# Kernel tuning notes

Measured on AMD Instinct MI355X. Metric: run time of the kernel, lower is better.

## Reference

```python
import jax, jax.numpy as jnp
import numpy as np

B, C, H = 256, 5, 13
N_AGENTS = 8192
N_EDGES = 262144
ACT = 21


def setup_inputs() -> dict:
    key = jax.random.key(0)
    ks = jax.random.split(key, 20)
    inp = {
        "x": jax.random.normal(ks[0], (B, C, H, H), jnp.float32),
        "x_msg": jax.random.normal(ks[1], (N_AGENTS,), jnp.float32),
        "edge_index": jax.random.randint(ks[2], (N_EDGES, 2), 0, N_AGENTS, jnp.int64 if jax.config.jax_enable_x64 else jnp.int32),
        "action": jax.random.randint(ks[3], (B,), 0, ACT, jnp.int32),
        # params (orthogonal init approximated by scaled normal; math identical)
        "conv1_w": jax.random.normal(ks[4], (32, 5, 3, 3), jnp.float32) * 0.1,
        "conv1_b": jnp.zeros((32,), jnp.float32),
        "conv2_w": jax.random.normal(ks[5], (64, 32, 3, 3), jnp.float32) * 0.05,
        "conv2_b": jnp.zeros((64,), jnp.float32),
        "fc_w": jax.random.normal(ks[6], (512, 1024), jnp.float32) * 0.03,
        "fc_b": jnp.zeros((512,), jnp.float32),
        "fc_mu_w": jax.random.normal(ks[7], (ACT, 512), jnp.float32) * 0.01,
        "fc_mu_b": jnp.zeros((ACT,), jnp.float32),
        "msg_w": jax.random.normal(ks[8], (N_AGENTS, 512), jnp.float32) * 0.01,
        "msg_b": jnp.zeros((N_AGENTS,), jnp.float32),
        "gcn1_w": jax.random.normal(ks[9], (2, 16), jnp.float32) * 0.5,
        "gcn1_b": jnp.zeros((16,), jnp.float32),
        "gcn2_w": jax.random.normal(ks[10], (16, N_AGENTS), jnp.float32) * 0.1,
        "gcn2_b": jnp.zeros((N_AGENTS,), jnp.float32),
    }
    return inp


def _gcn_norm(edge_index, n):
    # add self-loops; edge_index is (E,2) [src, dst]
    loops = jnp.arange(n, dtype=edge_index.dtype)
    src = jnp.concatenate([edge_index[:, 0], loops])
    dst = jnp.concatenate([edge_index[:, 1], loops])
    deg = jax.ops.segment_sum(jnp.ones_like(src, jnp.float32), dst, num_segments=n)
    dinv = jnp.where(deg > 0, jax.lax.rsqrt(deg), 0.0)
    norm = dinv[src] * dinv[dst]  # [E+n]
    return src, dst, norm


def _gcn_conv(h, src, dst, norm, W, b, n):
    hw = h @ W  # [n, out]
    out = jax.ops.segment_sum(norm[:, None] * hw[src], dst, num_segments=n)
    return out + b


def reference(x, x_msg, edge_index, action, conv1_w, conv1_b, conv2_w, conv2_b,
              fc_w, fc_b, fc_mu_w, fc_mu_b, msg_w, msg_b,
              gcn1_w, gcn1_b, gcn2_w, gcn2_b):
    dn = ("NCHW", "OIHW", "NCHW")
    h = jax.lax.conv_general_dilated(x, conv1_w, (2, 2), "VALID", dimension_numbers=dn)
    h = jax.nn.relu(h + conv1_b[None, :, None, None])  # [B,32,6,6]
    h = jax.lax.conv_general_dilated(h, conv2_w, (1, 1), "VALID", dimension_numbers=dn)
    h = jax.nn.relu(h + conv2_b[None, :, None, None])  # [B,64,4,4]
    h = h.reshape(h.shape[0], -1)  # [B,1024], torch NCHW flatten order
    hidden = jax.nn.relu(h @ fc_w.T + fc_b)  # [B,512]

    logits = hidden @ fc_mu_w.T + fc_mu_b            # [B,21]
    actor_encoding = hidden @ msg_w.T + msg_b        # [B,N]

    # Categorical log_prob / entropy for the given action
    logp = jax.nn.log_softmax(logits, axis=-1)
    log_prob = jnp.take_along_axis(logp, action[:, None], axis=1)[:, 0]
    entropy = -jnp.sum(jnp.exp(logp) * logp, axis=-1)

    # GNN message branch (eval mode: dropout is identity)
    feats = jnp.stack([x_msg, actor_encoding[0]], axis=0).T  # [N,2]
    n = feats.shape[0]
    src, dst, norm = _gcn_norm(edge_index, n)
    g = jax.nn.relu(_gcn_conv(feats, src, dst, norm, gcn1_w, gcn1_b, n))  # [N,16]
    g = _gcn_conv(g, src, dst, norm, gcn2_w, gcn2_b, n)                    # [N,N]
    msg_out = jax.nn.log_softmax(g, axis=1).mean(axis=1)                   # [N]

    return (action, msg_out, log_prob, entropy)
```

## Files before the change

kernel.cpp:

```cpp
#include <hip/hip_runtime.h>
#include <hip/hip_bf16.h>

#define NB 256
#define NACT 21
#define NA 8192
#define NE 262144
#define CSR_CAP 128
#define LOG2E 1.44269504f

#if __has_builtin(__builtin_amdgcn_exp2f)
#define EXP2F(x) __builtin_amdgcn_exp2f(x)
#else
#define EXP2F(x) exp2f(x)
#endif

typedef __attribute__((ext_vector_type(8))) short short8;
typedef __attribute__((ext_vector_type(4))) float float4v;

__device__ inline float wsum64(float v) {
#pragma unroll
  for (int m = 32; m > 0; m >>= 1) v += __shfl_xor(v, m, 64);
  return v;
}

__device__ inline unsigned short f2bf(float f) {
  union { __hip_bfloat16 h; unsigned short u; } cv;
  cv.h = __float2bfloat16(f);
  return cv.u;
}

__global__ __launch_bounds__(512, 2) void k_ip(
    const float* __restrict__ x, const float* __restrict__ c1w, const float* __restrict__ c1b_,
    const float* __restrict__ c2w, const float* __restrict__ fcw,
    const float* __restrict__ g2w, const float* __restrict__ g2b,
    unsigned short* c1b, unsigned short* w2abf, int* cnt,
    unsigned short* fcwbf, unsigned short* w2t, float* wpart) {
  __shared__ float sm[3437];
  int t = threadIdx.x, b = blockIdx.x;
  if (b >= 308) {
    float (*red)[17] = (float(*)[17])sm;
    float* b2s = sm + 272;
    int blk = b - 308;
    {
      int base = (blk * 512 + t) * 2;
      float2 v = *(const float2*)&fcw[base];
      fcwbf[base + 0] = f2bf(v.x);
      fcwbf[base + 1] = f2bf(v.y);
    }
    {
      if (t < 256) {
        int jj = t >> 4, k = t & 15;
        int j = blk * 16 + jj;
        float w = g2w[k * 8192 + j];
        w2t[j * 16 + k] = f2bf(w);
        red[jj][k] = w;
      }
      if (t < 16) b2s[t] = g2b[blk * 16 + t];
      __syncthreads();
      if (t < 16) {
        float s = 0.0f;
#pragma unroll
        for (int q = 0; q < 16; q++) s += red[q][t];
        wpart[blk * 17 + t] = s;
      } else if (t == 16) {
        float s = 0.0f;
#pragma unroll
        for (int q = 0; q < 16; q++) s += b2s[q];
        wpart[blk * 17 + 16] = s;
      }
    }
    return;
  }
  if (b >= 272) {
    int i = (b - 272) * 512 + t;
    w2abf[i] = f2bf(c2w[i]);
    return;
  }
  if (b >= 256) {
    cnt[(b - 256) * 512 + t] = 0;
    return;
  }
  float* xs = sm;
  float* w1s = sm + 845;
  float* c1s = sm + 2285;
  for (int i = t; i < 845; i += 512) xs[i] = x[b * 845 + i];
  for (int i = t; i < 1440; i += 512) w1s[i] = c1w[i];
  __syncthreads();
  for (int idx = t; idx < 1152; idx += 512) {
    int oc = idx / 36, p = idx - oc * 36;
    int oy = p / 6, ox = p - oy * 6;
    float acc = c1b_[oc];
    const float* wp = &w1s[oc * 45];
#pragma unroll
    for (int ic = 0; ic < 5; ic++)
#pragma unroll
      for (int ky = 0; ky < 3; ky++)
#pragma unroll
        for (int kx = 0; kx < 3; kx++)
          acc += xs[ic * 169 + (oy * 2 + ky) * 13 + ox * 2 + kx] * wp[ic * 9 + ky * 3 + kx];
    c1s[idx] = fmaxf(acc, 0.0f);
  }
  __syncthreads();
  for (int i = t; i < 4608; i += 512) {
    int p = i / 288, k = i - p * 288;
    int ic = k / 9, r = k - ic * 9;
    int ky = r / 3, kx = r - ky * 3;
    int oy = p >> 2, ox = p & 3;
    c1b[b * 4608 + i] = f2bf(c1s[ic * 36 + (oy + ky) * 6 + ox + kx]);
  }
}

__global__ __launch_bounds__(512, 2) void k_cf(
    const int* __restrict__ edges, int* cnt, int* csr,
    const unsigned short* __restrict__ c1b, const unsigned short* __restrict__ w2abf,
    const float* __restrict__ c2b, const unsigned short* __restrict__ fcwbf,
    const float* __restrict__ fcb, const float* __restrict__ wpart,
    float* hidden, float* wsf) {
  __shared__ __align__(16) unsigned short hs[16384];
  __shared__ __align__(16) unsigned short w2a[18432];
  __shared__ float red[2048];
  int t = threadIdx.x, blk = blockIdx.x;
  int wave = t >> 6, lane = t & 63;
  int m = lane & 15, quad = lane >> 4;
  if (blk >= 1024) {
    if (t < 272) {
      int q = t / 17, c = t - q * 17;
      float s = 0.0f;
      for (int r = q; r < 512; r += 16) s += wpart[r * 17 + c];
      red[t] = s;
    }
    __syncthreads();
    if (t < 17) {
      float s = 0.0f;
#pragma unroll
      for (int q = 0; q < 16; q++) s += red[q * 17 + t];
      wsf[t] = s;
    }
    return;
  }
  if (blk >= 512) {
    int e = (blk - 512) * 512 + t;
    int s = edges[2 * e], d = edges[2 * e + 1];
    int slot = atomicAdd(&cnt[d], 1);
    if (slot < CSR_CAP) csr[d * CSR_CAP + slot] = s;
    return;
  }
  for (int i = t; i < 2304; i += 512)
    *(short8*)&w2a[i * 8] = *(const short8*)&w2abf[i * 8];
  __syncthreads();
  int tr = blk >> 5, tc = blk & 31;
  {
    int nlb = wave * 32;
    int nbase = tr * 256 + nlb;
    float4v z = {0.0f, 0.0f, 0.0f, 0.0f};
    float4v acc00 = z, acc01 = z, acc02 = z, acc03 = z;
    float4v acc10 = z, acc11 = z, acc12 = z, acc13 = z;
#pragma unroll
    for (int ks = 0; ks < 9; ks++) {
      int ko = ks * 32 + quad * 8;
      short8 a0 = *(const short8*)&w2a[(0 * 16 + m) * 288 + ko];
      short8 a1 = *(const short8*)&w2a[(1 * 16 + m) * 288 + ko];
      short8 a2 = *(const short8*)&w2a[(2 * 16 + m) * 288 + ko];
      short8 a3 = *(const short8*)&w2a[(3 * 16 + m) * 288 + ko];
      short8 b0 = *(const short8*)&c1b[(nbase + m) * 288 + ko];
      short8 b1 = *(const short8*)&c1b[(nbase + 16 + m) * 288 + ko];
      acc00 = __builtin_amdgcn_mfma_f32_16x16x32_bf16(a0, b0, acc00, 0, 0, 0);
      acc01 = __builtin_amdgcn_mfma_f32_16x16x32_bf16(a1, b0, acc01, 0, 0, 0);
      acc02 = __builtin_amdgcn_mfma_f32_16x16x32_bf16(a2, b0, acc02, 0, 0, 0);
      acc03 = __builtin_amdgcn_mfma_f32_16x16x32_bf16(a3, b0, acc03, 0, 0, 0);
      acc10 = __builtin_amdgcn_mfma_f32_16x16x32_bf16(a0, b1, acc10, 0, 0, 0);
      acc11 = __builtin_amdgcn_mfma_f32_16x16x32_bf16(a1, b1, acc11, 0, 0, 0);
      acc12 = __builtin_amdgcn_mfma_f32_16x16x32_bf16(a2, b1, acc12, 0, 0, 0);
      acc13 = __builtin_amdgcn_mfma_f32_16x16x32_bf16(a3, b1, acc13, 0, 0, 0);
    }
    float4v accs[2][4] = {{acc00, acc01, acc02, acc03}, {acc10, acc11, acc12, acc13}};
#pragma unroll
    for (int nt = 0; nt < 2; nt++) {
#pragma unroll
      for (int mt = 0; mt < 4; mt++) {
#pragma unroll
        for (int r = 0; r < 4; r++) {
          int oc = mt * 16 + quad * 4 + r;
          int nl = nlb + nt * 16 + m;
          hs[(nl >> 4) * 1024 + oc * 16 + (nl & 15)] =
              f2bf(fmaxf(accs[nt][mt][r] + c2b[oc], 0.0f));
        }
      }
    }
  }
  __syncthreads();
  {
    const unsigned short* ap = &hs[m * 1024 + wave * 128 + quad * 8];
    const unsigned short* bp = &fcwbf[(tc * 16 + m) * 1024 + wave * 128 + quad * 8];
    float4v acc = {0.0f, 0.0f, 0.0f, 0.0f};
#pragma unroll
    for (int ks = 0; ks < 4; ks++) {
      short8 av = *(const short8*)(ap + ks * 32);
      short8 bv = *(const short8*)(bp + ks * 32);
      acc = __builtin_amdgcn_mfma_f32_16x16x32_bf16(av, bv, acc, 0, 0, 0);
    }
#pragma unroll
    for (int r = 0; r < 4; r++) red[wave * 256 + (quad * 4 + r) * 16 + m] = acc[r];
    __syncthreads();
    if (t < 256) {
      float s = 0.0f;
#pragma unroll
      for (int w = 0; w < 8; w++) s += red[w * 256 + t];
      int gr = tr * 16 + (t >> 4);
      int gc = tc * 16 + (t & 15);
      hidden[gr * 512 + gc] = fmaxf(s + fcb[gc], 0.0f);
    }
  }
}

__global__ __launch_bounds__(512, 2) void k_he(
    const float* __restrict__ hidden, const float* __restrict__ muw,
    const float* __restrict__ mub, const float* __restrict__ msgw,
    const float* __restrict__ msgb, const int* __restrict__ cnt,
    const float* __restrict__ x_msg, const int* __restrict__ action,
    float2* xe, float* dinv, float* out) {
  __shared__ float muT[10752];
  __shared__ float hrows[2048];
  int t = threadIdx.x, blk = blockIdx.x;
  int wave = t >> 6, lane = t & 63;
  if (blk >= 512) {
    int i = (blk - 512) * 512 + t;
    float d = rsqrtf((float)cnt[i] + 1.0f);
    dinv[i] = d;
    xe[i].x = d * x_msg[i];
    return;
  }
  if (blk < 64) {
    int b0 = blk * 4;
    for (int i = t; i < 10752; i += 512) {
      int a = i >> 9, k = i & 511;
      muT[k * 21 + a] = muw[i];
    }
    for (int i = t; i < 2048; i += 512) hrows[i] = hidden[b0 * 512 + i];
    __syncthreads();
    if (wave < 4) {
      int b = b0 + wave;
      float logit = -1e30f;
      if (lane < NACT) {
        float acc = mub[lane];
        const float* hr = &hrows[wave * 512];
        for (int k = 0; k < 512; k++) acc += hr[k] * muT[k * 21 + lane];
        logit = acc;
      }
      float mx = logit;
#pragma unroll
      for (int s = 32; s > 0; s >>= 1) mx = fmaxf(mx, __shfl_xor(mx, s, 64));
      float e = (lane < NACT) ? __expf(logit - mx) : 0.0f;
      float se = wsum64(e);
      float swl = wsum64(e * logit);
      float lse = mx + __logf(se);
      int act = action[b];
      if (lane == 0) {
        out[b] = (float)act;
        out[8704 + b] = lse - swl / se;
      }
      if (lane == act) out[8448 + b] = logit - lse;
    }
  } else {
    int wg = (blk - 64) * 8 + wave;
    for (int j = wg; j < NA; j += 3584) {
      const float* wp = &msgw[j * 512 + lane * 8];
      float4 w0 = *(const float4*)(wp);
      float4 w1 = *(const float4*)(wp + 4);
      float4 h0 = *(const float4*)&hidden[lane * 8];
      float4 h1 = *(const float4*)&hidden[lane * 8 + 4];
      float s = w0.x * h0.x + w0.y * h0.y + w0.z * h0.z + w0.w * h0.w +
                w1.x * h1.x + w1.y * h1.y + w1.z * h1.z + w1.w * h1.w;
      s = wsum64(s);
      if (lane == 0) xe[j].y = rsqrtf((float)cnt[j] + 1.0f) * (s + msgb[j]);
    }
  }
}

__global__ __launch_bounds__(512, 4) void k_g1(
    const int* __restrict__ cnt, const int* __restrict__ csr,
    const float* __restrict__ dinv, const float2* __restrict__ xe,
    const float* __restrict__ g1w, const float* __restrict__ g1b, float* gbuf2) {
  int t = threadIdx.x, blk = blockIdx.x;
  int wave = t >> 6, lane = t & 63;
  int wg = blk * 8 + wave;
#pragma unroll
  for (int rr = 0; rr < 2; rr++) {
    int i = wg * 2 + rr;
    int ci = min(cnt[i], CSR_CAP);
    float di = dinv[i];
    float a0 = 0.0f, a1 = 0.0f;
    for (int e = lane; e < ci; e += 64) {
      int s = csr[i * CSR_CAP + e];
      float2 v = xe[s];
      a0 += v.x;
      a1 += v.y;
    }
    float2 vi = xe[i];
    float f0 = (wsum64(a0) + vi.x) * di;
    float f1 = (wsum64(a1) + vi.y) * di;
    if (lane < 16) {
      float gv = fmaxf(f0 * g1w[lane] + f1 * g1w[16 + lane] + g1b[lane], 0.0f);
      gbuf2[i * 16 + lane] = di * gv;
    }
  }
}

__global__ __launch_bounds__(512, 2) void k_msg(
    const int* __restrict__ cnt, const int* __restrict__ csr,
    const float* __restrict__ dinv, const float* __restrict__ gbuf2,
    const float* __restrict__ wsf, const unsigned short* __restrict__ w2t,
    const float* __restrict__ g2b, float* out) {
  __shared__ __align__(16) unsigned short vbf[256];
  __shared__ float vf[256];
  __shared__ float pl[2048];
  __shared__ float sl[128];
  __shared__ float wsfs[17];
  int t = threadIdx.x, blk = blockIdx.x;
  int wave = t >> 6, lane = t & 63;
  int rowbase = blk * 16;
  if (t < 17) wsfs[t] = wsf[t];
  {
    int eq = lane >> 4, c = lane & 15;
#pragma unroll
    for (int rr = 0; rr < 2; rr++) {
      int il = wave * 2 + rr;
      int i = rowbase + il;
      int ci = min(cnt[i], CSR_CAP);
      float di = dinv[i];
      float acc = (eq == 0) ? gbuf2[i * 16 + c] : 0.0f;
      for (int e = eq; e < ci; e += 4) {
        int s = csr[i * CSR_CAP + e];
        acc += gbuf2[s * 16 + c];
      }
      acc *= di;
      acc += __shfl_xor(acc, 16, 64);
      acc += __shfl_xor(acc, 32, 64);
      if (eq == 0) {
        vf[il * 16 + c] = acc;
        vbf[il * 16 + c] = f2bf(acc * LOG2E);
      }
    }
  }
  __syncthreads();
  float myMean = 0.0f;
  if (t < 16) {
    float dot = 0.0f;
#pragma unroll
    for (int c = 0; c < 16; c++) dot += vf[t * 16 + c] * wsfs[c];
    myMean = (dot + wsfs[16]) * (1.0f / 8192.0f);
  }
  {
    int quad = lane >> 4, n = lane & 15;
    int k8 = quad * 8;
    short8 za = {0, 0, 0, 0, 0, 0, 0, 0};
    short8 a1 = za;
    if (quad < 2) a1 = *(const short8*)&vbf[n * 16 + k8];
    float sacc[4];
#pragma unroll
    for (int q = 0; q < 4; q++) sacc[q] = 0.0f;
    int colb = wave * 1024 + n;
    for (int tp = 0; tp < 64; tp += 2) {
      int col1 = colb + tp * 16;
      int col2 = col1 + 16;
      short8 b1 = za, b2 = za;
      if (quad < 2) {
        b1 = *(const short8*)&w2t[col1 * 16 + k8];
        b2 = *(const short8*)&w2t[col2 * 16 + k8];
      }
      float bb1 = g2b[col1] * LOG2E, bb2 = g2b[col2] * LOG2E;
      float4v c1 = {bb1, bb1, bb1, bb1};
      float4v c2 = {bb2, bb2, bb2, bb2};
      float4v s11 = __builtin_amdgcn_mfma_f32_16x16x32_bf16(a1, b1, c1, 0, 0, 0);
      float4v s12 = __builtin_amdgcn_mfma_f32_16x16x32_bf16(a1, b2, c2, 0, 0, 0);
#pragma unroll
      for (int r = 0; r < 4; r++) sacc[r] += EXP2F(s11[r]) + EXP2F(s12[r]);
    }
#pragma unroll
    for (int q = 0; q < 4; q++) {
      int rl = quad * 4 + q;
      pl[rl * 128 + wave * 16 + n] = sacc[q];
    }
  }
  __syncthreads();
  if (t < 128) {
    int r = t >> 3, seg = t & 7;
    int base = r * 128 + seg * 16;
    float ll = 0.0f;
#pragma unroll
    for (int i = 0; i < 16; i++) ll += pl[base + i];
    sl[r * 8 + seg] = ll;
  }
  __syncthreads();
  if (t < 16) {
    float ll = 0.0f;
#pragma unroll
    for (int i = 0; i < 8; i++) ll += sl[t * 8 + i];
    out[256 + rowbase + t] = myMean - __logf(ll);
  }
}

extern "C" void kernel_launch(void* const* d_in, const int* in_sizes, int n_in,
                              void* d_out, int out_size, void* d_ws, size_t ws_size,
                              hipStream_t stream) {
  const float* x     = (const float*)d_in[0];
  const float* x_msg = (const float*)d_in[1];
  const int*   edges = (const int*)d_in[2];
  const int*   action= (const int*)d_in[3];
  const float* c1w   = (const float*)d_in[4];
  const float* c1bb  = (const float*)d_in[5];
  const float* c2w   = (const float*)d_in[6];
  const float* c2b   = (const float*)d_in[7];
  const float* fcw   = (const float*)d_in[8];
  const float* fcb   = (const float*)d_in[9];
  const float* muw   = (const float*)d_in[10];
  const float* mub   = (const float*)d_in[11];
  const float* msgw  = (const float*)d_in[12];
  const float* msgb  = (const float*)d_in[13];
  const float* g1w   = (const float*)d_in[14];
  const float* g1b   = (const float*)d_in[15];
  const float* g2w   = (const float*)d_in[16];
  const float* g2b   = (const float*)d_in[17];
  float* out = (float*)d_out;

  float* ws     = (float*)d_ws;
  unsigned short* fcwbf   = (unsigned short*)(ws + 131072);
  float* hidden = ws + 393216;
  float2* xe    = (float2*)(ws + 524288);
  float* dinv   = ws + 540672;
  float* gbuf2  = ws + 548864;
  float* wpart  = ws + 679936;
  unsigned short* w2t = (unsigned short*)(ws + 688640);
  int*   cnt    = (int*)(ws + 754176);
  int*   csr    = (int*)(ws + 762368);
  float* wsf    = ws + 1810944;
  unsigned short* c1b   = (unsigned short*)(ws + 1810964);
  unsigned short* w2abf = (unsigned short*)(ws + 2400788);

  k_ip <<<820, 512, 0, stream>>>(x, c1w, c1bb, c2w, fcw, g2w, g2b,
                                 c1b, w2abf, cnt, fcwbf, w2t, wpart);
  k_cf <<<1025, 512, 0, stream>>>(edges, cnt, csr, c1b, w2abf, c2b,
                                  fcwbf, fcb, wpart, hidden, wsf);
  k_he <<<528, 512, 0, stream>>>(hidden, muw, mub, msgw, msgb, cnt, x_msg,
                                 action, xe, dinv, out);
  k_g1 <<<512, 512, 0, stream>>>(cnt, csr, dinv, xe, g1w, g1b, gbuf2);
  k_msg<<<512, 512, 0, stream>>>(cnt, csr, dinv, gbuf2, wsf, w2t, g2b, out);
}
```

Measured before the change: 172.1 us.

## Fuse kernels: early CSR build, recompute batch-0 hidden for message branch, persistent counters

```diff
diff --git a/kernel.cpp b/kernel.cpp
--- a/kernel.cpp
+++ b/kernel.cpp
@@ -17,6 +17,8 @@
 typedef __attribute__((ext_vector_type(8))) short short8;
 typedef __attribute__((ext_vector_type(4))) float float4v;
 
+__device__ int g_cnt[NA];
+
 __device__ inline float wsum64(float v) {
 #pragma unroll
   for (int m = 32; m > 0; m >>= 1) v += __shfl_xor(v, m, 64);
@@ -31,16 +33,28 @@
 
 __global__ __launch_bounds__(512, 2) void k_ip(
     const float* __restrict__ x, const float* __restrict__ c1w, const float* __restrict__ c1b_,
-    const float* __restrict__ c2w, const float* __restrict__ fcw,
-    const float* __restrict__ g2w, const float* __restrict__ g2b,
-    unsigned short* c1b, unsigned short* w2abf, int* cnt,
-    unsigned short* fcwbf, unsigned short* w2t, float* wpart) {
-  __shared__ float sm[3437];
+    const float* __restrict__ c2w, const float* __restrict__ c2b, const float* __restrict__ fcw,
+    const float* __restrict__ g2w, const float* __restrict__ g2b, const int* __restrict__ edges,
+    unsigned short* c1b, unsigned short* w2abf, int* csr,
+    unsigned short* fcwbf, unsigned short* w2t, float* wpart, float* h0p) {
+  __shared__ float sm[3565];
   int t = threadIdx.x, b = blockIdx.x;
-  if (b >= 308) {
+  if (b >= 256 && b < 768) {
+    int e = (b - 256) * 512 + t;
+    int s = edges[2 * e], d = edges[2 * e + 1];
+    int slot = atomicAdd(&g_cnt[d], 1);
+    if (slot < CSR_CAP) csr[d * CSR_CAP + slot] = s;
+    return;
+  }
+  if (b >= 768 && b < 804) {
+    int i = (b - 768) * 512 + t;
+    w2abf[i] = f2bf(c2w[i]);
+    return;
+  }
+  if (b >= 804 && b < 1316) {
     float (*red)[17] = (float(*)[17])sm;
     float* b2s = sm + 272;
-    int blk = b - 308;
+    int blk = b - 804;
     {
       int base = (blk * 512 + t) * 2;
       float2 v = *(const float2*)&fcw[base];
@@ -71,19 +85,12 @@
     }
     return;
   }
-  if (b >= 272) {
-    int i = (b - 272) * 512 + t;
-    w2abf[i] = f2bf(c2w[i]);
-    return;
-  }
-  if (b >= 256) {
-    cnt[(b - 256) * 512 + t] = 0;
-    return;
-  }
+  int img = (b < 256) ? b : 0;
   float* xs = sm;
   float* w1s = sm + 845;
   float* c1s = sm + 2285;
-  for (int i = t; i < 845; i += 512) xs[i] = x[b * 845 + i];
+  float* h0s = sm + 3437;
+  for (int i = t; i < 845; i += 512) xs[i] = x[img * 845 + i];
   for (int i = t; i < 1440; i += 512) w1s[i] = c1w[i];
   __syncthreads();
   for (int idx = t; idx < 1152; idx += 512) {
@@ -101,28 +108,59 @@
     c1s[idx] = fmaxf(acc, 0.0f);
   }
   __syncthreads();
-  for (int i = t; i < 4608; i += 512) {
-    int p = i / 288, k = i - p * 288;
-    int ic = k / 9, r = k - ic * 9;
-    int ky = r / 3, kx = r - ky * 3;
-    int oy = p >> 2, ox = p & 3;
-    c1b[b * 4608 + i] = f2bf(c1s[ic * 36 + (oy + ky) * 6 + ox + kx]);
+  if (b < 256) {
+    for (int i = t; i < 4608; i += 512) {
+      int p = i / 288, k = i - p * 288;
+      int ic = k / 9, r = k - ic * 9;
+      int ky = r / 3, kx = r - ky * 3;
+      int oy = p >> 2, ox = p & 3;
+      c1b[b * 4608 + i] = f2bf(c1s[ic * 36 + (oy + ky) * 6 + ox + kx]);
+    }
+    return;
+  }
+  int q = b - 1316;
+  if (t < 128) {
+    int ocl = t >> 4, pos = t & 15;
+    int oc = q * 8 + ocl;
+    int oy = pos >> 2, ox = pos & 3;
+    float acc = c2b[oc];
+    const float* wp = &c2w[oc * 288];
+#pragma unroll
+    for (int ic = 0; ic < 32; ic++)
+#pragma unroll
+      for (int ky = 0; ky < 3; ky++)
+#pragma unroll
+        for (int kx = 0; kx < 3; kx++)
+          acc += c1s[ic * 36 + (oy + ky) * 6 + ox + kx] * wp[ic * 9 + ky * 3 + kx];
+    h0s[t] = fmaxf(acc, 0.0f);
+  }
+  __syncthreads();
+  {
+    float p = 0.0f;
+    const float* fr = &fcw[t * 1024 + q * 128];
+#pragma unroll 4
+    for (int j = 0; j < 128; j += 4) {
+      float4 f4 = *(const float4*)&fr[j];
+      p += f4.x * h0s[j] + f4.y * h0s[j + 1] + f4.z * h0s[j + 2] + f4.w * h0s[j + 3];
+    }
+    h0p[q * 512 + t] = p;
   }
 }
 
 __global__ __launch_bounds__(512, 2) void k_cf(
-    const int* __restrict__ edges, int* cnt, int* csr,
     const unsigned short* __restrict__ c1b, const unsigned short* __restrict__ w2abf,
     const float* __restrict__ c2b, const unsigned short* __restrict__ fcwbf,
     const float* __restrict__ fcb, const float* __restrict__ wpart,
-    float* hidden, float* wsf) {
+    const float* __restrict__ h0p, const float* __restrict__ msgw,
+    const float* __restrict__ msgb, const float* __restrict__ x_msg,
+    float* hidden, float* wsf, float2* xe, float* dinv) {
   __shared__ __align__(16) unsigned short hs[16384];
   __shared__ __align__(16) unsigned short w2a[18432];
   __shared__ float red[2048];
   int t = threadIdx.x, blk = blockIdx.x;
   int wave = t >> 6, lane = t & 63;
   int m = lane & 15, quad = lane >> 4;
-  if (blk >= 1024) {
+  if (blk == 512) {
     if (t < 272) {
       int q = t / 17, c = t - q * 17;
       float s = 0.0f;
@@ -138,11 +176,32 @@
     }
     return;
   }
-  if (blk >= 512) {
-    int e = (blk - 512) * 512 + t;
-    int s = edges[2 * e], d = edges[2 * e + 1];
-    int slot = atomicAdd(&cnt[d], 1);
-    if (slot < CSR_CAP) csr[d * CSR_CAP + slot] = s;
+  if (blk >= 513) {
+    float h0f[8];
+#pragma unroll
+    for (int q2 = 0; q2 < 8; q2++) {
+      int c = lane * 8 + q2;
+      float v = fcb[c];
+#pragma unroll
+      for (int q = 0; q < 8; q++) v += h0p[q * 512 + c];
+      h0f[q2] = fmaxf(v, 0.0f);
+    }
+    int j0 = (blk - 513) * 16 + wave * 2;
+#pragma unroll
+    for (int rr = 0; rr < 2; rr++) {
+      int j = j0 + rr;
+      const float* wp = &msgw[j * 512 + lane * 8];
+      float4 w0 = *(const float4*)(wp);
+      float4 w1 = *(const float4*)(wp + 4);
+      float s = w0.x * h0f[0] + w0.y * h0f[1] + w0.z * h0f[2] + w0.w * h0f[3] +
+                w1.x * h0f[4] + w1.y * h0f[5] + w1.z * h0f[6] + w1.w * h0f[7];
+      s = wsum64(s);
+      if (lane == 0) {
+        float dj = rsqrtf((float)g_cnt[j] + 1.0f);
+        dinv[j] = dj;
+        xe[j] = make_float2(dj * x_msg[j], dj * (s + msgb[j]));
+      }
+    }
     return;
   }
   for (int i = t; i < 2304; i += 512)
@@ -213,23 +272,16 @@
   }
 }
 
-__global__ __launch_bounds__(512, 2) void k_he(
+__global__ __launch_bounds__(512, 2) void k_hg(
     const float* __restrict__ hidden, const float* __restrict__ muw,
-    const float* __restrict__ mub, const float* __restrict__ msgw,
-    const float* __restrict__ msgb, const int* __restrict__ cnt,
-    const float* __restrict__ x_msg, const int* __restrict__ action,
-    float2* xe, float* dinv, float* out) {
+    const float* __restrict__ mub, const int* __restrict__ action,
+    const int* __restrict__ csr, const float* __restrict__ dinv,
+    const float2* __restrict__ xe, const float* __restrict__ g1w,
+    const float* __restrict__ g1b, float* gbuf2, float* out) {
   __shared__ float muT[10752];
   __shared__ float hrows[2048];
   int t = threadIdx.x, blk = blockIdx.x;
   int wave = t >> 6, lane = t & 63;
-  if (blk >= 512) {
-    int i = (blk - 512) * 512 + t;
-    float d = rsqrtf((float)cnt[i] + 1.0f);
-    dinv[i] = d;
-    xe[i].x = d * x_msg[i];
-    return;
-  }
   if (blk < 64) {
     int b0 = blk * 4;
     for (int i = t; i < 10752; i += 512) {
@@ -263,54 +315,33 @@
     }
   } else {
     int wg = (blk - 64) * 8 + wave;
-    for (int j = wg; j < NA; j += 3584) {
-      const float* wp = &msgw[j * 512 + lane * 8];
-      float4 w0 = *(const float4*)(wp);
-      float4 w1 = *(const float4*)(wp + 4);
-      float4 h0 = *(const float4*)&hidden[lane * 8];
-      float4 h1 = *(const float4*)&hidden[lane * 8 + 4];
-      float s = w0.x * h0.x + w0.y * h0.y + w0.z * h0.z + w0.w * h0.w +
-                w1.x * h1.x + w1.y * h1.y + w1.z * h1.z + w1.w * h1.w;
-      s = wsum64(s);
-      if (lane == 0) xe[j].y = rsqrtf((float)cnt[j] + 1.0f) * (s + msgb[j]);
-    }
-  }
-}
-
-__global__ __launch_bounds__(512, 4) void k_g1(
-    const int* __restrict__ cnt, const int* __restrict__ csr,
-    const float* __restrict__ dinv, const float2* __restrict__ xe,
-    const float* __restrict__ g1w, const float* __restrict__ g1b, float* gbuf2) {
-  int t = threadIdx.x, blk = blockIdx.x;
-  int wave = t >> 6, lane = t & 63;
-  int wg = blk * 8 + wave;
-#pragma unroll
-  for (int rr = 0; rr < 2; rr++) {
-    int i = wg * 2 + rr;
-    int ci = min(cnt[i], CSR_CAP);
-    float di = dinv[i];
-    float a0 = 0.0f, a1 = 0.0f;
-    for (int e = lane; e < ci; e += 64) {
-      int s = csr[i * CSR_CAP + e];
-      float2 v = xe[s];
-      a0 += v.x;
-      a1 += v.y;
-    }
-    float2 vi = xe[i];
-    float f0 = (wsum64(a0) + vi.x) * di;
-    float f1 = (wsum64(a1) + vi.y) * di;
-    if (lane < 16) {
-      float gv = fmaxf(f0 * g1w[lane] + f1 * g1w[16 + lane] + g1b[lane], 0.0f);
-      gbuf2[i * 16 + lane] = di * gv;
+#pragma unroll
+    for (int rr = 0; rr < 2; rr++) {
+      int i = wg * 2 + rr;
+      int ci = min(g_cnt[i], CSR_CAP);
+      float di = dinv[i];
+      float a0 = 0.0f, a1 = 0.0f;
+      for (int e = lane; e < ci; e += 64) {
+        int s = csr[i * CSR_CAP + e];
+        float2 v = xe[s];
+        a0 += v.x;
+        a1 += v.y;
+      }
+      float2 vi = xe[i];
+      float f0 = (wsum64(a0) + vi.x) * di;
+      float f1 = (wsum64(a1) + vi.y) * di;
+      if (lane < 16) {
+        float gv = fmaxf(f0 * g1w[lane] + f1 * g1w[16 + lane] + g1b[lane], 0.0f);
+        gbuf2[i * 16 + lane] = di * gv;
+      }
     }
   }
 }
 
 __global__ __launch_bounds__(512, 2) void k_msg(
-    const int* __restrict__ cnt, const int* __restrict__ csr,
-    const float* __restrict__ dinv, const float* __restrict__ gbuf2,
-    const float* __restrict__ wsf, const unsigned short* __restrict__ w2t,
-    const float* __restrict__ g2b, float* out) {
+    const int* __restrict__ csr, const float* __restrict__ dinv,
+    const float* __restrict__ gbuf2, const float* __restrict__ wsf,
+    const unsigned short* __restrict__ w2t, const float* __restrict__ g2b, float* out) {
   __shared__ __align__(16) unsigned short vbf[256];
   __shared__ float vf[256];
   __shared__ float pl[2048];
@@ -326,7 +357,7 @@
     for (int rr = 0; rr < 2; rr++) {
       int il = wave * 2 + rr;
       int i = rowbase + il;
-      int ci = min(cnt[i], CSR_CAP);
+      int ci = min(g_cnt[i], CSR_CAP);
       float di = dinv[i];
       float acc = (eq == 0) ? gbuf2[i * 16 + c] : 0.0f;
       for (int e = eq; e < ci; e += 4) {
@@ -398,6 +429,7 @@
     for (int i = 0; i < 8; i++) ll += sl[t * 8 + i];
     out[256 + rowbase + t] = myMean - __logf(ll);
   }
+  if (t < 16) g_cnt[rowbase + t] = 0;
 }
 
 extern "C" void kernel_launch(void* const* d_in, const int* in_sizes, int n_in,
@@ -431,18 +463,17 @@
   float* gbuf2  = ws + 548864;
   float* wpart  = ws + 679936;
   unsigned short* w2t = (unsigned short*)(ws + 688640);
-  int*   cnt    = (int*)(ws + 754176);
   int*   csr    = (int*)(ws + 762368);
   float* wsf    = ws + 1810944;
   unsigned short* c1b   = (unsigned short*)(ws + 1810964);
   unsigned short* w2abf = (unsigned short*)(ws + 2400788);
-
-  k_ip <<<820, 512, 0, stream>>>(x, c1w, c1bb, c2w, fcw, g2w, g2b,
-                                 c1b, w2abf, cnt, fcwbf, w2t, wpart);
-  k_cf <<<1025, 512, 0, stream>>>(edges, cnt, csr, c1b, w2abf, c2b,
-                                  fcwbf, fcb, wpart, hidden, wsf);
-  k_he <<<528, 512, 0, stream>>>(hidden, muw, mub, msgw, msgb, cnt, x_msg,
-                                 action, xe, dinv, out);
-  k_g1 <<<512, 512, 0, stream>>>(cnt, csr, dinv, xe, g1w, g1b, gbuf2);
-  k_msg<<<512, 512, 0, stream>>>(cnt, csr, dinv, gbuf2, wsf, w2t, g2b, out);
-}
+  float* h0p    = ws + 2410004;
+
+  k_ip <<<1324, 512, 0, stream>>>(x, c1w, c1bb, c2w, c2b, fcw, g2w, g2b, edges,
+                                  c1b, w2abf, csr, fcwbf, w2t, wpart, h0p);
+  k_cf <<<1025, 512, 0, stream>>>(c1b, w2abf, c2b, fcwbf, fcb, wpart, h0p,
+                                  msgw, msgb, x_msg, hidden, wsf, xe, dinv);
+  k_hg <<<576, 512, 0, stream>>>(hidden, muw, mub, action, csr, dinv, xe,
+                                 g1w, g1b, gbuf2, out);
+  k_msg<<<512, 512, 0, stream>>>(csr, dinv, gbuf2, wsf, w2t, g2b, out);
+}
```

Result: slower. 186.1 us (+8.1%).
